# Kernel optimization log

Hardware: AMD Instinct MI355X
Metric: run time of the kernel (lower is better)

The kernel has to match this reference:

```python
import jax, jax.numpy as jnp
import numpy as np

B = 4096      # graphs
N = 21        # nodes per graph (EEG electrodes)
CIN = 512
H1 = 1024
H2 = 1024
COUT = 512
R = 4         # SE reduction
RANK = 10     # nodevec rank
EPS = 1e-5
THRESH = 0.1


def setup_inputs() -> dict:
    key = jax.random.key(0)
    ks = jax.random.split(key, 16)
    p = lambda i, shape, s=0.02: (jax.random.normal(ks[i], shape, jnp.float32) * s)
    return {
        "x": jax.random.normal(ks[0], (B * N, CIN), jnp.float32),
        "batch": jnp.arange(B * N, dtype=jnp.int32) // N,
        "nodevec1": jax.random.normal(ks[1], (N, RANK), jnp.float32),
        "nodevec2": jax.random.normal(ks[2], (RANK, N), jnp.float32),
        "se_w1": p(3, (CIN, CIN // R), 0.05),
        "se_w2": p(4, (CIN // R, CIN), 0.05),
        "W1": p(5, (CIN, H1)), "b1": jnp.zeros((H1,), jnp.float32),
        "W2": p(6, (H1, H2)), "b2": jnp.zeros((H2,), jnp.float32),
        "W3": p(7, (H2, COUT)), "b3": jnp.zeros((COUT,), jnp.float32),
        "bn1_g": jnp.ones((H1,), jnp.float32), "bn1_b": jnp.zeros((H1,), jnp.float32),
        "bn2_g": jnp.ones((H2,), jnp.float32), "bn2_b": jnp.zeros((H2,), jnp.float32),
        "bn3_g": jnp.ones((COUT,), jnp.float32), "bn3_b": jnp.zeros((COUT,), jnp.float32),
        "rs1_w": p(8, (CIN, H1)), "rs1_b": jnp.zeros((H1,), jnp.float32),
        "fc_w": p(9, (COUT, 2 * COUT)), "fc_b": jnp.zeros((2 * COUT,), jnp.float32),
    }


def _batchnorm(h, g, b):
    # training-mode BN: biased batch stats over the node dimension
    m = h.mean(0)
    v = h.var(0)
    return (h - m) * jax.lax.rsqrt(v + EPS) * g + b


def _gcn(A, h, W, b):
    # GCNConv with precomputed normalized+thresholded weights:
    # out = A_block_diag @ (h @ W) + b, done densely per graph since A is 21x21
    hm = (h @ W).reshape(B, N, -1)                 # [B, N, Cout]
    agg = jnp.einsum('ij,bjc->bic', A, hm)         # message passing per graph
    return agg.reshape(B * N, -1) + b


def _forward(x, batch, nodevec1, nodevec2, se_w1, se_w2,
             W1, b1, W2, b2, W3, b3,
             bn1_g, bn1_b, bn2_g, bn2_b, bn3_g, bn3_b,
             rs1_w, rs1_b, fc_w, fc_b):
    # SE layer on [B, N, C]: channel-wise gating from node-mean features
    x3 = x.reshape(B, N, CIN)
    y = jax.nn.sigmoid(jax.nn.relu(x3.mean(1) @ se_w1) @ se_w2)   # [B, C]
    xg = (x3 * y[:, None, :]).reshape(B * N, CIN)
    # adaptive adjacency: sigmoid(nv1 @ nv2), symmetric normalize, threshold
    adp = jax.nn.sigmoid(nodevec1 @ nodevec2)                      # [N, N]
    at = adp + jnp.eye(N, dtype=adp.dtype)
    deg = at.sum(1)
    dinv = jnp.where(deg > 0, deg ** -0.5, 0.0)
    A = dinv[:, None] * at * dinv[None, :]
    A = jnp.where(A > THRESH, A, 0.0)
    # layer 1 (+ projected residual, BN, relu; dropout omitted = eval)
    h = _batchnorm(_gcn(A, xg, W1, b1), bn1_g, bn1_b) + (xg @ rs1_w + rs1_b)
    h = jax.nn.relu(h)
    # layer 2 (h1 == h2 -> identity residual)
    h = jax.nn.relu(_batchnorm(_gcn(A, h, W2, b2), bn2_g, bn2_b) + h)
    # layer 3
    h = _batchnorm(_gcn(A, h, W3, b3), bn3_g, bn3_b)
    # global mean pool by graph id
    ssum = jax.ops.segment_sum(h, batch, num_segments=B)
    cnt = jax.ops.segment_sum(jnp.ones((h.shape[0], 1), h.dtype), batch, num_segments=B)
    pooled = ssum / cnt
    return pooled @ fc_w + fc_b                                    # [B, 2*COUT]


def reference(x, batch, nodevec1, nodevec2, se_w1, se_w2,
              W1, b1, W2, b2, W3, b3,
              bn1_g, bn1_b, bn2_g, bn2_b, bn3_g, bn3_b,
              rs1_w, rs1_b, fc_w, fc_b):
    return _forward(x, batch, nodevec1, nodevec2, se_w1, se_w2,
                    W1, b1, W2, b2, W3, b3,
                    bn1_g, bn1_b, bn2_g, bn2_b, bn3_g, bn3_b,
                    rs1_w, rs1_b, fc_w, fc_b)
```

## Files before the change

kernel.cpp:

```cpp
#include <hip/hip_runtime.h>

typedef _Float16 f16;
typedef f16 f16x2 __attribute__((ext_vector_type(2)));
typedef f16 f16x8 __attribute__((ext_vector_type(8)));
typedef float f32x4 __attribute__((ext_vector_type(4)));
typedef const void __attribute__((address_space(1)))* gas1;
typedef void __attribute__((address_space(3)))* las3;

#define NB 4096
#define NN 21
#define MROWS (NB*NN)
#define CIN 512

__global__ void k_adj(const float* __restrict__ nv1, const float* __restrict__ nv2,
                      float* __restrict__ Aout) {
  __shared__ float at[21][21];
  __shared__ float dinv[21];
  int t = threadIdx.x;
  if (t < 441) {
    int i = t / 21, j = t % 21;
    float s = 0.f;
    #pragma unroll
    for (int r = 0; r < 10; r++) s += nv1[i*10 + r] * nv2[r*21 + j];
    float v = 1.f / (1.f + expf(-s));
    if (i == j) v += 1.f;
    at[i][j] = v;
  }
  __syncthreads();
  if (t < 21) {
    float d = 0.f;
    #pragma unroll
    for (int j = 0; j < 21; j++) d += at[t][j];
    dinv[t] = d > 0.f ? rsqrtf(d) : 0.f;
  }
  __syncthreads();
  if (t < 441) {
    int i = t / 21, j = t % 21;
    float a = dinv[i] * at[i][j] * dinv[j];
    Aout[t] = a > 0.1f ? a : 0.f;
  }
}

__global__ void k_transpose(const float* __restrict__ src, f16* __restrict__ dst,
                            int K, int N) {
  __shared__ float tile[32][33];
  int n0 = blockIdx.x * 32, k0 = blockIdx.y * 32;
  int tx = threadIdx.x, ty = threadIdx.y;
  #pragma unroll
  for (int i = 0; i < 4; i++)
    tile[ty + 8*i][tx] = src[(size_t)(k0 + ty + 8*i) * N + n0 + tx];
  __syncthreads();
  #pragma unroll
  for (int i = 0; i < 4; i++)
    dst[(size_t)(n0 + ty + 8*i) * K + k0 + tx] = (f16)tile[tx][ty + 8*i];
}

__global__ void k_mean(const float* __restrict__ x, float* __restrict__ xm) {
  int b = blockIdx.x, t = threadIdx.x;
  for (int c = t; c < CIN; c += 256) {
    float s = 0.f;
    #pragma unroll
    for (int n = 0; n < NN; n++) s += x[((size_t)b*NN + n)*CIN + c];
    xm[(size_t)b*CIN + c] = s * (1.f/21.f);
  }
}

__global__ void k_se1(const float* __restrict__ xm, const float* __restrict__ w1,
                      float* __restrict__ y1) {
  __shared__ float row[CIN];
  int b = blockIdx.x, t = threadIdx.x;
  for (int k = t; k < CIN; k += 128) row[k] = xm[(size_t)b*CIN + k];
  __syncthreads();
  float acc = 0.f;
  for (int k = 0; k < CIN; k++) acc += row[k] * w1[(size_t)k*128 + t];
  y1[(size_t)b*128 + t] = fmaxf(acc, 0.f);
}

__global__ void k_se2(const float* __restrict__ y1, const float* __restrict__ w2,
                      float* __restrict__ y) {
  __shared__ float row[128];
  int b = blockIdx.x, t = threadIdx.x;
  if (t < 128) row[t] = y1[(size_t)b*128 + t];
  __syncthreads();
  float acc = 0.f;
  for (int k = 0; k < 128; k++) acc += row[k] * w2[(size_t)k*CIN + t];
  y[(size_t)b*CIN + t] = 1.f / (1.f + expf(-acc));
}

__global__ void k_gate(const float* __restrict__ x, const float* __restrict__ y,
                       f16* __restrict__ xg) {
  size_t i8 = (size_t)blockIdx.x * 256 + threadIdx.x;
  size_t base = i8 * 8;
  int r = (int)(base >> 9);
  int c = (int)(base & 511);
  int b = r / 21;
  const float4* xp = (const float4*)(x + base);
  const float4* yp = (const float4*)(y + (size_t)b*CIN + c);
  float4 a0 = xp[0], a1 = xp[1];
  float4 g0 = yp[0], g1 = yp[1];
  f16x8 o;
  o[0] = (f16)(a0.x * g0.x); o[1] = (f16)(a0.y * g0.y);
  o[2] = (f16)(a0.z * g0.z); o[3] = (f16)(a0.w * g0.w);
  o[4] = (f16)(a1.x * g1.x); o[5] = (f16)(a1.y * g1.y);
  o[6] = (f16)(a1.z * g1.z); o[7] = (f16)(a1.w * g1.w);
  *(f16x8*)(xg + base) = o;
}

#define GBM 128
#define GBN 256
#define BUFB 49152

template<int MODE>
__global__ __launch_bounds__(512, 1)
void k_gemm8(const f16* __restrict__ A, const f16* __restrict__ BT,
             f16* __restrict__ C1, const float* __restrict__ bias,
             float* __restrict__ Cf, float* __restrict__ psum,
             float* __restrict__ psq, int N, int K, int lgn) {
  __shared__ __align__(16) char lds[3 * BUFB];
  const int tid = threadIdx.x;
  const int nwg = gridDim.x;
  const int g = blockIdx.x;
  const int swz = (g & 7) * (nwg >> 3) + (g >> 3);
  const int bn = swz & ((1 << lgn) - 1);
  const int bm = swz >> lgn;
  const int lane = tid & 63;
  const int wid = tid >> 6;
  const int wr = wid >> 2;
  const int wc = wid & 3;
  const int fr = lane & 15;
  const int kg = lane >> 4;

  size_t srcOff[6]; int ldsOff[6];
  #pragma unroll
  for (int j = 0; j < 6; j++) {
    int gid = j * 512 + tid;
    if (gid < 1024) {
      int row = gid >> 3, gr = gid & 7;
      int gsw = gr ^ (row & 7);
      srcOff[j] = (size_t)(bm * GBM + row) * K + gsw * 8;
      ldsOff[j] = gid * 16;
    } else {
      int bgid = gid - 1024;
      int row = bgid >> 3, gr = bgid & 7;
      int gsw = gr ^ (row & 7);
      srcOff[j] = (size_t)(bn * GBN + row) * K + gsw * 8;
      ldsOff[j] = 16384 + bgid * 16;
    }
  }

  int aOff[4], axor[4], bOff[4], bxor[4];
  #pragma unroll
  for (int m = 0; m < 4; m++) {
    int row = wr*64 + m*16 + fr;
    aOff[m] = row * 128; axor[m] = row & 7;
  }
  #pragma unroll
  for (int n = 0; n < 4; n++) {
    int row = wc*64 + n*16 + fr;
    bOff[n] = 16384 + row * 128; bxor[n] = row & 7;
  }

  f32x4 acc[4][4];
  #pragma unroll
  for (int m = 0; m < 4; m++)
    #pragma unroll
    for (int n = 0; n < 4; n++)
      #pragma unroll
      for (int r = 0; r < 4; r++) acc[m][n][r] = 0.f;

  auto STAGE3 = [&](int t2, int sbuf, int j0) {
    char* dst = (char*)lds + sbuf * BUFB;
    const size_t kof = (size_t)t2 * 64;
    #pragma unroll
    for (int j = 0; j < 3; j++) {
      int jj = j0 + j;
      const f16* src = (jj < 2 ? A : BT) + srcOff[jj] + kof;
      __builtin_amdgcn_global_load_lds((gas1)src, (las3)(dst + ldsOff[jj]), 16, 0, 0);
    }
  };
  auto READF = [&](f16x8* avv, f16x8* bvv, const char* rb, int s) {
    #pragma unroll
    for (int m = 0; m < 4; m++)
      avv[m] = *(const f16x8*)(rb + aOff[m] + (((s*4 + kg) ^ axor[m]) << 4));
    #pragma unroll
    for (int n = 0; n < 4; n++)
      bvv[n] = *(const f16x8*)(rb + bOff[n] + (((s*4 + kg) ^ bxor[n]) << 4));
  };

  f16x8 av0[4], bv0[4], av1[4], bv1[4];
  const int NT = K >> 6;
  STAGE3(0, 0, 0); STAGE3(0, 0, 3);
  STAGE3(1, 1, 0); STAGE3(1, 1, 3);
  asm volatile("s_waitcnt vmcnt(6)" ::: "memory");
  asm volatile("s_barrier" ::: "memory");
  READF(av0, bv0, (const char*)lds, 0);

  for (int t = 0; t < NT; t++) {
    const char* rb  = (const char*)lds + (t % 3) * BUFB;
    const char* rbn = (const char*)lds + ((t + 1) % 3) * BUFB;
    const int sb = (t + 2) % 3;
    const bool stg  = (t + 2) < NT;
    const bool more = (t + 1) < NT;

    if (stg) STAGE3(t + 2, sb, 0);
    READF(av1, bv1, rb, 1);
    __builtin_amdgcn_s_setprio(1);
    #pragma unroll
    for (int m = 0; m < 4; m++)
      #pragma unroll
      for (int n = 0; n < 4; n++)
        acc[m][n] = __builtin_amdgcn_mfma_f32_16x16x32_f16(av0[m], bv0[n], acc[m][n], 0, 0, 0);
    __builtin_amdgcn_s_setprio(0);
    if (stg) STAGE3(t + 2, sb, 3);

    if (more) {
      if (stg) asm volatile("s_waitcnt vmcnt(6)" ::: "memory");
      else     asm volatile("s_waitcnt vmcnt(0)" ::: "memory");
      asm volatile("s_barrier" ::: "memory");
      READF(av0, bv0, rbn, 0);
    }
    __builtin_amdgcn_s_setprio(1);
    #pragma unroll
    for (int m = 0; m < 4; m++)
      #pragma unroll
      for (int n = 0; n < 4; n++)
        acc[m][n] = __builtin_amdgcn_mfma_f32_16x16x32_f16(av1[m], bv1[n], acc[m][n], 0, 0, 0);
    __builtin_amdgcn_s_setprio(0);
    asm volatile("s_barrier" ::: "memory");
  }

  const int crow = bm * GBM + wr * 64 + ((lane >> 4) << 2);
  const int ccol = bn * GBN + wc * 64 + fr;
  if constexpr (MODE == 2) {
    #pragma unroll
    for (int n = 0; n < 4; n++) {
      float bb = bias[ccol + n*16];
      #pragma unroll
      for (int m = 0; m < 4; m++)
        #pragma unroll
        for (int r = 0; r < 4; r++)
          Cf[(size_t)(crow + m*16 + r) * N + (ccol + n*16)] = acc[m][n][r] + bb;
    }
  } else {
    #pragma unroll
    for (int m = 0; m < 4; m++)
      #pragma unroll
      for (int n = 0; n < 4; n++)
        #pragma unroll
        for (int r = 0; r < 4; r++)
          C1[(size_t)(crow + m*16 + r) * N + (ccol + n*16)] = (f16)acc[m][n][r];
  }
  if constexpr (MODE == 1) {
    float s[4], q[4];
    #pragma unroll
    for (int n = 0; n < 4; n++) {
      float ss = 0.f, qq = 0.f;
      #pragma unroll
      for (int m = 0; m < 4; m++)
        #pragma unroll
        for (int r = 0; r < 4; r++) { float v = acc[m][n][r]; ss += v; qq = fmaf(v, v, qq); }
      s[n] = ss; q[n] = qq;
    }
    #pragma unroll
    for (int n = 0; n < 4; n++) {
      s[n] += __shfl_xor(s[n], 16); s[n] += __shfl_xor(s[n], 32);
      q[n] += __shfl_xor(q[n], 16); q[n] += __shfl_xor(q[n], 32);
    }
    float* wred = (float*)lds;
    if ((lane >> 4) == 0) {
      #pragma unroll
      for (int n = 0; n < 4; n++) {
        wred[wr*256 + wc*64 + n*16 + fr]       = s[n];
        wred[512 + wr*256 + wc*64 + n*16 + fr] = q[n];
      }
    }
    __syncthreads();
    if (tid < 256) {
      psum[(size_t)bm * N + bn*256 + tid] = wred[tid]       + wred[256 + tid];
      psq [(size_t)bm * N + bn*256 + tid] = wred[512 + tid] + wred[768 + tid];
    }
  }
}

__global__ __launch_bounds__(256)
void k_mixip(f16* __restrict__ t, const float* __restrict__ Aadj) {
  __shared__ float A[441];
  int b = blockIdx.x, tid = threadIdx.x;
  for (int i = tid; i < 441; i += 256) A[i] = Aadj[i];
  __syncthreads();
  int c0 = tid * 2;
  size_t base = (size_t)b * NN * 512 + c0;
  float vx[21], vy[21];
  #pragma unroll
  for (int j = 0; j < 21; j++) {
    f16x2 v = *(const f16x2*)(t + base + (size_t)j * 512);
    vx[j] = (float)v[0]; vy[j] = (float)v[1];
  }
  #pragma unroll
  for (int i = 0; i < 21; i++) {
    float a0 = 0.f, a1 = 0.f;
    #pragma unroll
    for (int j = 0; j < 21; j++) { float w = A[i*21+j]; a0 = fmaf(w, vx[j], a0); a1 = fmaf(w, vy[j], a1); }
    f16x2 o; o[0] = (f16)a0; o[1] = (f16)a1;
    *(f16x2*)(t + base + (size_t)i * 512) = o;
  }
}

__global__ __launch_bounds__(256)
void k_mix(f16* __restrict__ t, const float* __restrict__ Aadj,
           float* __restrict__ psum, float* __restrict__ psq, int C) {
  __shared__ float A[441];
  int b = blockIdx.x, tid = threadIdx.x;
  for (int i = tid; i < 441; i += 256) A[i] = Aadj[i];
  __syncthreads();
  int c0 = (blockIdx.y * 256 + tid) * 2;
  size_t base = (size_t)b * NN * C + c0;
  float vx[21], vy[21];
  #pragma unroll
  for (int j = 0; j < 21; j++) {
    f16x2 v = *(const f16x2*)(t + base + (size_t)j * C);
    vx[j] = (float)v[0]; vy[j] = (float)v[1];
  }
  float s0 = 0.f, s1 = 0.f, q0 = 0.f, q1 = 0.f;
  #pragma unroll
  for (int i = 0; i < 21; i++) {
    float a0 = 0.f, a1 = 0.f;
    #pragma unroll
    for (int j = 0; j < 21; j++) {
      float w = A[i*21 + j];
      a0 = fmaf(w, vx[j], a0);
      a1 = fmaf(w, vy[j], a1);
    }
    f16x2 o; o[0] = (f16)a0; o[1] = (f16)a1;
    *(f16x2*)(t + base + (size_t)i * C) = o;
    s0 += a0; s1 += a1;
    q0 = fmaf(a0, a0, q0); q1 = fmaf(a1, a1, q1);
  }
  float2 sv; sv.x = s0; sv.y = s1;
  float2 qv; qv.x = q0; qv.y = q1;
  *(float2*)(psum + (size_t)b * C + c0) = sv;
  *(float2*)(psq  + (size_t)b * C + c0) = qv;
}

__global__ void k_reduce(const float* __restrict__ ps, const float* __restrict__ pq,
                         float* __restrict__ rs, float* __restrict__ rq,
                         int C, int per) {
  int c = blockIdx.x * 256 + threadIdx.x;
  int py = blockIdx.y;
  float s = 0.f, q = 0.f;
  for (int p = py*per; p < py*per + per; p++) {
    s += ps[(size_t)p*C + c];
    q += pq[(size_t)p*C + c];
  }
  rs[(size_t)py*C + c] = s;
  rq[(size_t)py*C + c] = q;
}

__global__ void k_bnparams(const float* __restrict__ psum, const float* __restrict__ psq,
                           const float* __restrict__ gamma, const float* __restrict__ beta,
                           const float* __restrict__ resbias,
                           float* __restrict__ scale, float* __restrict__ shift,
                           int C, int npart) {
  int c = blockIdx.x * 256 + threadIdx.x;
  float s = 0.f, q = 0.f;
  for (int p = 0; p < npart; p++) { s += psum[(size_t)p*C + c]; q += psq[(size_t)p*C + c]; }
  const float Minv = 1.f / (float)MROWS;
  float mean = s * Minv;
  float var = q * Minv - mean * mean;
  float sc = gamma[c] * rsqrtf(var + 1e-5f);
  float sh = beta[c] - mean * sc;
  if (resbias) sh += resbias[c];
  scale[c] = sc; shift[c] = sh;
}

__global__ void k_finalize(const f16* __restrict__ g, const f16* res,
                           f16* dst, const float* __restrict__ scale,
                           const float* __restrict__ shift, int cmask) {
  size_t i8 = (size_t)blockIdx.x * 256 + threadIdx.x;
  size_t base = i8 * 8;
  int c = (int)(base & (size_t)cmask);
  f16x8 gv = *(const f16x8*)(g + base);
  f16x8 rv = *(const f16x8*)(res + base);
  f16x8 o;
  #pragma unroll
  for (int j = 0; j < 8; j++) {
    float v = (float)gv[j] * scale[c + j] + shift[c + j] + (float)rv[j];
    o[j] = (f16)fmaxf(v, 0.f);
  }
  *(f16x8*)(dst + base) = o;
}

__global__ __launch_bounds__(256)
void k_finmix(const f16* t, const f16* res, f16* hout, f16* hmix,
              const float* __restrict__ scale, const float* __restrict__ shift,
              const float* __restrict__ Aadj, int C) {
  __shared__ float A[441];
  int b = blockIdx.x, tid = threadIdx.x;
  for (int i = tid; i < 441; i += 256) A[i] = Aadj[i];
  __syncthreads();
  int c0 = (blockIdx.y * 256 + tid) * 2;
  float scx = scale[c0], scy = scale[c0+1];
  float shx = shift[c0], shy = shift[c0+1];
  size_t base = (size_t)b * NN * C + c0;
  float hx[21], hy[21];
  #pragma unroll
  for (int j = 0; j < 21; j++) {
    f16x2 tv = *(const f16x2*)(t + base + (size_t)j*C);
    f16x2 rv = *(const f16x2*)(res + base + (size_t)j*C);
    hx[j] = fmaxf((float)tv[0]*scx + shx + (float)rv[0], 0.f);
    hy[j] = fmaxf((float)tv[1]*scy + shy + (float)rv[1], 0.f);
    if (hout) {
      f16x2 o; o[0] = (f16)hx[j]; o[1] = (f16)hy[j];
      *(f16x2*)(hout + base + (size_t)j*C) = o;
    }
  }
  #pragma unroll
  for (int i = 0; i < 21; i++) {
    float a0 = 0.f, a1 = 0.f;
    #pragma unroll
    for (int j = 0; j < 21; j++) { float w = A[i*21+j]; a0 = fmaf(w, hx[j], a0); a1 = fmaf(w, hy[j], a1); }
    f16x2 o; o[0] = (f16)a0; o[1] = (f16)a1;
    *(f16x2*)(hmix + base + (size_t)i*C) = o;
  }
}

__global__ void k_pool(const f16* __restrict__ g3, const float* __restrict__ scale,
                       const float* __restrict__ shift, f16* __restrict__ pooled) {
  int b = blockIdx.x, t = threadIdx.x;
  for (int c = t; c < 512; c += 256) {
    float s = 0.f;
    #pragma unroll
    for (int n = 0; n < NN; n++) s += (float)g3[((size_t)b*NN + n)*512 + c];
    pooled[(size_t)b*512 + c] = (f16)((s * (1.f/21.f)) * scale[c] + shift[c]);
  }
}

extern "C" void kernel_launch(void* const* d_in, const int* in_sizes, int n_in,
                              void* d_out, int out_size, void* d_ws, size_t ws_size,
                              hipStream_t stream) {
  const float* x     = (const float*)d_in[0];
  const float* nv1   = (const float*)d_in[2];
  const float* nv2   = (const float*)d_in[3];
  const float* se_w1 = (const float*)d_in[4];
  const float* se_w2 = (const float*)d_in[5];
  const float* W1    = (const float*)d_in[6];
  const float* W2    = (const float*)d_in[8];
  const float* W3    = (const float*)d_in[10];
  const float* bn1g  = (const float*)d_in[12];
  const float* bn1b  = (const float*)d_in[13];
  const float* bn2g  = (const float*)d_in[14];
  const float* bn2b  = (const float*)d_in[15];
  const float* bn3g  = (const float*)d_in[16];
  const float* bn3b  = (const float*)d_in[17];
  const float* rs1w  = (const float*)d_in[18];
  const float* rs1b  = (const float*)d_in[19];
  const float* fcw   = (const float*)d_in[20];
  const float* fcb   = (const float*)d_in[21];
  float* out = (float*)d_out;

  char* ws = (char*)d_ws;
  size_t off = 0;
  auto alloc = [&](size_t bytes) -> char* {
    char* p = ws + off;
    off = (off + bytes + 255) & ~(size_t)255;
    return p;
  };

  float* A_adj = (float*)alloc(441 * 4);
  f16* W1T  = (f16*)alloc((size_t)1024 * 512 * 2);
  f16* RS1T = (f16*)alloc((size_t)1024 * 512 * 2);
  f16* W2T  = (f16*)alloc((size_t)1024 * 1024 * 2);
  f16* W3T  = (f16*)alloc((size_t)512 * 1024 * 2);
  f16* FCWT = (f16*)alloc((size_t)1024 * 512 * 2);
  float* psum = (float*)alloc((size_t)NB * 1024 * 4);
  float* psq  = (float*)alloc((size_t)NB * 1024 * 4);
  float* y1   = (float*)alloc((size_t)NB * 128 * 4);
  float* rsum = (float*)alloc((size_t)32 * 1024 * 4);
  float* rsq  = (float*)alloc((size_t)32 * 1024 * 4);
  float* sc1 = (float*)alloc(1024 * 4);
  float* sh1 = (float*)alloc(1024 * 4);
  float* sc2 = (float*)alloc(1024 * 4);
  float* sh2 = (float*)alloc(1024 * 4);
  float* sc3 = (float*)alloc(1024 * 4);
  float* sh3 = (float*)alloc(1024 * 4);
  f16* pooled = (f16*)alloc((size_t)NB * 512 * 2);
  f16* G = (f16*)alloc((size_t)MROWS * 512 * 2);
  f16* R = (f16*)alloc((size_t)MROWS * 1024 * 2);
  f16* T = (f16*)alloc((size_t)MROWS * 1024 * 2);
  float* xm = psum;
  float* yv = psq;
  (void)ws_size; (void)in_sizes; (void)n_in; (void)out_size;

  k_adj<<<1, 512, 0, stream>>>(nv1, nv2, A_adj);
  k_transpose<<<dim3(32, 16), dim3(32, 8), 0, stream>>>(W1,   W1T,  512, 1024);
  k_transpose<<<dim3(32, 16), dim3(32, 8), 0, stream>>>(rs1w, RS1T, 512, 1024);
  k_transpose<<<dim3(32, 32), dim3(32, 8), 0, stream>>>(W2,   W2T,  1024, 1024);
  k_transpose<<<dim3(16, 32), dim3(32, 8), 0, stream>>>(W3,   W3T,  1024, 512);
  k_transpose<<<dim3(32, 16), dim3(32, 8), 0, stream>>>(fcw,  FCWT, 512, 1024);

  k_mean<<<NB, 256, 0, stream>>>(x, xm);
  k_se1<<<NB, 128, 0, stream>>>(xm, se_w1, y1);
  k_se2<<<NB, 512, 0, stream>>>(y1, se_w2, yv);
  k_gate<<<21504, 256, 0, stream>>>(x, yv, G);

  k_gemm8<0><<<672*4, 512, 0, stream>>>(G, RS1T, R, nullptr, nullptr, nullptr, nullptr, 1024, 512, 2);
  k_mixip<<<NB, 256, 0, stream>>>(G, A_adj);
  k_gemm8<1><<<672*4, 512, 0, stream>>>(G, W1T, T, nullptr, nullptr, psum, psq, 1024, 512, 2);
  k_reduce<<<dim3(4, 32), 256, 0, stream>>>(psum, psq, rsum, rsq, 1024, 21);
  k_bnparams<<<4, 256, 0, stream>>>(rsum, rsq, bn1g, bn1b, rs1b, sc1, sh1, 1024, 32);
  k_finalize<<<43008, 256, 0, stream>>>(T, R, R, sc1, sh1, 1023);

  k_gemm8<0><<<672*4, 512, 0, stream>>>(R, W2T, T, nullptr, nullptr, nullptr, nullptr, 1024, 1024, 2);
  k_mix<<<dim3(NB, 2), 256, 0, stream>>>(T, A_adj, psum, psq, 1024);
  k_reduce<<<dim3(4, 32), 256, 0, stream>>>(psum, psq, rsum, rsq, 1024, 128);
  k_bnparams<<<4, 256, 0, stream>>>(rsum, rsq, bn2g, bn2b, nullptr, sc2, sh2, 1024, 32);
  k_finmix<<<dim3(NB, 2), 256, 0, stream>>>(T, R, nullptr, T, sc2, sh2, A_adj, 1024);

  k_gemm8<1><<<672*2, 512, 0, stream>>>(T, W3T, G, nullptr, nullptr, psum, psq, 512, 1024, 1);
  k_reduce<<<dim3(2, 32), 256, 0, stream>>>(psum, psq, rsum, rsq, 512, 21);
  k_bnparams<<<2, 256, 0, stream>>>(rsum, rsq, bn3g, bn3b, nullptr, sc3, sh3, 512, 32);

  k_pool<<<NB, 256, 0, stream>>>(G, sc3, sh3, pooled);
  k_gemm8<2><<<32*4, 512, 0, stream>>>(pooled, FCWT, nullptr, fcb, out, nullptr, nullptr, 1024, 512, 2);
}
```

Before: 1.186 ms.

## Shrink GEMM tiles to 128x128 with 4 waves, double buffering and two workgroups per CU

The f16 MFMA GEMM changes from a 128x256 tile run by 8 waves with a triple-buffered LDS pipeline and one workgroup per CU to a 128x128 tile run by 4 waves. It uses a 64 KB double buffer and launch bounds that allow two workgroups per CU. The aim is to let co-resident workgroups hide each other's load and barrier stalls and to balance the grid better. In exchange, each tile reuses operands less, and each k-step now waits for all outstanding loads, so the pipeline inside a workgroup is shallower. The grid sizes, swizzle shift and BN partial-sum reduction layout are adjusted to the new tile width.

Result: slower. 1.214 ms (+2.4%).

```diff
diff --git a/kernel.cpp b/kernel.cpp
--- a/kernel.cpp
+++ b/kernel.cpp
@@ -107,16 +107,16 @@
 }
 
 #define GBM 128
-#define GBN 256
-#define BUFB 49152
+#define GBN 128
+#define HBUF 32768
 
 template<int MODE>
-__global__ __launch_bounds__(512, 1)
-void k_gemm8(const f16* __restrict__ A, const f16* __restrict__ BT,
+__global__ __launch_bounds__(256, 2)
+void k_gemm4(const f16* __restrict__ A, const f16* __restrict__ BT,
              f16* __restrict__ C1, const float* __restrict__ bias,
              float* __restrict__ Cf, float* __restrict__ psum,
              float* __restrict__ psq, int N, int K, int lgn) {
-  __shared__ __align__(16) char lds[3 * BUFB];
+  __shared__ __align__(16) char lds[2 * HBUF];
   const int tid = threadIdx.x;
   const int nwg = gridDim.x;
   const int g = blockIdx.x;
@@ -125,26 +125,24 @@
   const int bm = swz >> lgn;
   const int lane = tid & 63;
   const int wid = tid >> 6;
-  const int wr = wid >> 2;
-  const int wc = wid & 3;
+  const int wr = wid >> 1;
+  const int wc = wid & 1;
   const int fr = lane & 15;
   const int kg = lane >> 4;
 
-  size_t srcOff[6]; int ldsOff[6];
-  #pragma unroll
-  for (int j = 0; j < 6; j++) {
-    int gid = j * 512 + tid;
+  size_t srcOff[8]; int ldsOff[8];
+  #pragma unroll
+  for (int j = 0; j < 8; j++) {
+    int gid = j * 256 + tid;
+    int row = (gid >> 3) & 127;
+    int gr = gid & 7;
+    int gsw = gr ^ (row & 7);
     if (gid < 1024) {
-      int row = gid >> 3, gr = gid & 7;
-      int gsw = gr ^ (row & 7);
       srcOff[j] = (size_t)(bm * GBM + row) * K + gsw * 8;
       ldsOff[j] = gid * 16;
     } else {
-      int bgid = gid - 1024;
-      int row = bgid >> 3, gr = bgid & 7;
-      int gsw = gr ^ (row & 7);
       srcOff[j] = (size_t)(bn * GBN + row) * K + gsw * 8;
-      ldsOff[j] = 16384 + bgid * 16;
+      ldsOff[j] = 16384 + (gid - 1024) * 16;
     }
   }
 
@@ -168,14 +166,13 @@
       #pragma unroll
       for (int r = 0; r < 4; r++) acc[m][n][r] = 0.f;
 
-  auto STAGE3 = [&](int t2, int sbuf, int j0) {
-    char* dst = (char*)lds + sbuf * BUFB;
+  auto STAGE8 = [&](int t2, int sbuf) {
+    char* dst = (char*)lds + sbuf * HBUF;
     const size_t kof = (size_t)t2 * 64;
     #pragma unroll
-    for (int j = 0; j < 3; j++) {
-      int jj = j0 + j;
-      const f16* src = (jj < 2 ? A : BT) + srcOff[jj] + kof;
-      __builtin_amdgcn_global_load_lds((gas1)src, (las3)(dst + ldsOff[jj]), 16, 0, 0);
+    for (int j = 0; j < 8; j++) {
+      const f16* src = (j < 4 ? A : BT) + srcOff[j] + kof;
+      __builtin_amdgcn_global_load_lds((gas1)src, (las3)(dst + ldsOff[j]), 16, 0, 0);
     }
   };
   auto READF = [&](f16x8* avv, f16x8* bvv, const char* rb, int s) {
@@ -189,20 +186,17 @@
 
   f16x8 av0[4], bv0[4], av1[4], bv1[4];
   const int NT = K >> 6;
-  STAGE3(0, 0, 0); STAGE3(0, 0, 3);
-  STAGE3(1, 1, 0); STAGE3(1, 1, 3);
-  asm volatile("s_waitcnt vmcnt(6)" ::: "memory");
+  STAGE8(0, 0);
+  asm volatile("s_waitcnt vmcnt(0)" ::: "memory");
   asm volatile("s_barrier" ::: "memory");
   READF(av0, bv0, (const char*)lds, 0);
 
   for (int t = 0; t < NT; t++) {
-    const char* rb  = (const char*)lds + (t % 3) * BUFB;
-    const char* rbn = (const char*)lds + ((t + 1) % 3) * BUFB;
-    const int sb = (t + 2) % 3;
-    const bool stg  = (t + 2) < NT;
-    const bool more = (t + 1) < NT;
-
-    if (stg) STAGE3(t + 2, sb, 0);
+    const char* rb  = (const char*)lds + (t & 1) * HBUF;
+    const char* rbn = (const char*)lds + ((t + 1) & 1) * HBUF;
+    const bool stg = (t + 1) < NT;
+
+    if (stg) STAGE8(t + 1, (t + 1) & 1);
     READF(av1, bv1, rb, 1);
     __builtin_amdgcn_s_setprio(1);
     #pragma unroll
@@ -211,14 +205,9 @@
       for (int n = 0; n < 4; n++)
         acc[m][n] = __builtin_amdgcn_mfma_f32_16x16x32_f16(av0[m], bv0[n], acc[m][n], 0, 0, 0);
     __builtin_amdgcn_s_setprio(0);
-    if (stg) STAGE3(t + 2, sb, 3);
-
-    if (more) {
-      if (stg) asm volatile("s_waitcnt vmcnt(6)" ::: "memory");
-      else     asm volatile("s_waitcnt vmcnt(0)" ::: "memory");
-      asm volatile("s_barrier" ::: "memory");
-      READF(av0, bv0, rbn, 0);
-    }
+    if (stg) asm volatile("s_waitcnt vmcnt(0)" ::: "memory");
+    asm volatile("s_barrier" ::: "memory");
+    if (stg) READF(av0, bv0, rbn, 0);
     __builtin_amdgcn_s_setprio(1);
     #pragma unroll
     for (int m = 0; m < 4; m++)
@@ -226,7 +215,6 @@
       for (int n = 0; n < 4; n++)
         acc[m][n] = __builtin_amdgcn_mfma_f32_16x16x32_f16(av1[m], bv1[n], acc[m][n], 0, 0, 0);
     __builtin_amdgcn_s_setprio(0);
-    asm volatile("s_barrier" ::: "memory");
   }
 
   const int crow = bm * GBM + wr * 64 + ((lane >> 4) << 2);
@@ -267,17 +255,18 @@
       q[n] += __shfl_xor(q[n], 16); q[n] += __shfl_xor(q[n], 32);
     }
     float* wred = (float*)lds;
+    __syncthreads();
     if ((lane >> 4) == 0) {
       #pragma unroll
       for (int n = 0; n < 4; n++) {
-        wred[wr*256 + wc*64 + n*16 + fr]       = s[n];
-        wred[512 + wr*256 + wc*64 + n*16 + fr] = q[n];
+        wred[wr*128 + wc*64 + n*16 + fr]       = s[n];
+        wred[256 + wr*128 + wc*64 + n*16 + fr] = q[n];
       }
     }
     __syncthreads();
-    if (tid < 256) {
-      psum[(size_t)bm * N + bn*256 + tid] = wred[tid]       + wred[256 + tid];
-      psq [(size_t)bm * N + bn*256 + tid] = wred[512 + tid] + wred[768 + tid];
+    if (tid < 128) {
+      psum[(size_t)bm * N + bn*128 + tid] = wred[tid]       + wred[128 + tid];
+      psq [(size_t)bm * N + bn*128 + tid] = wred[256 + tid] + wred[384 + tid];
     }
   }
 }
@@ -503,23 +492,23 @@
   k_se2<<<NB, 512, 0, stream>>>(y1, se_w2, yv);
   k_gate<<<21504, 256, 0, stream>>>(x, yv, G);
 
-  k_gemm8<0><<<672*4, 512, 0, stream>>>(G, RS1T, R, nullptr, nullptr, nullptr, nullptr, 1024, 512, 2);
+  k_gemm4<0><<<672*8, 256, 0, stream>>>(G, RS1T, R, nullptr, nullptr, nullptr, nullptr, 1024, 512, 3);
   k_mixip<<<NB, 256, 0, stream>>>(G, A_adj);
-  k_gemm8<1><<<672*4, 512, 0, stream>>>(G, W1T, T, nullptr, nullptr, psum, psq, 1024, 512, 2);
+  k_gemm4<1><<<672*8, 256, 0, stream>>>(G, W1T, T, nullptr, nullptr, psum, psq, 1024, 512, 3);
   k_reduce<<<dim3(4, 32), 256, 0, stream>>>(psum, psq, rsum, rsq, 1024, 21);
   k_bnparams<<<4, 256, 0, stream>>>(rsum, rsq, bn1g, bn1b, rs1b, sc1, sh1, 1024, 32);
   k_finalize<<<43008, 256, 0, stream>>>(T, R, R, sc1, sh1, 1023);
 
-  k_gemm8<0><<<672*4, 512, 0, stream>>>(R, W2T, T, nullptr, nullptr, nullptr, nullptr, 1024, 1024, 2);
+  k_gemm4<0><<<672*8, 256, 0, stream>>>(R, W2T, T, nullptr, nullptr, nullptr, nullptr, 1024, 1024, 3);
   k_mix<<<dim3(NB, 2), 256, 0, stream>>>(T, A_adj, psum, psq, 1024);
   k_reduce<<<dim3(4, 32), 256, 0, stream>>>(psum, psq, rsum, rsq, 1024, 128);
   k_bnparams<<<4, 256, 0, stream>>>(rsum, rsq, bn2g, bn2b, nullptr, sc2, sh2, 1024, 32);
   k_finmix<<<dim3(NB, 2), 256, 0, stream>>>(T, R, nullptr, T, sc2, sh2, A_adj, 1024);
 
-  k_gemm8<1><<<672*2, 512, 0, stream>>>(T, W3T, G, nullptr, nullptr, psum, psq, 512, 1024, 1);
+  k_gemm4<1><<<672*4, 256, 0, stream>>>(T, W3T, G, nullptr, nullptr, psum, psq, 512, 1024, 2);
   k_reduce<<<dim3(2, 32), 256, 0, stream>>>(psum, psq, rsum, rsq, 512, 21);
   k_bnparams<<<2, 256, 0, stream>>>(rsum, rsq, bn3g, bn3b, nullptr, sc3, sh3, 512, 32);
 
   k_pool<<<NB, 256, 0, stream>>>(G, sc3, sh3, pooled);
-  k_gemm8<2><<<32*4, 512, 0, stream>>>(pooled, FCWT, nullptr, fcb, out, nullptr, nullptr, 1024, 512, 2);
-}
+  k_gemm4<2><<<32*8, 256, 0, stream>>>(pooled, FCWT, nullptr, fcb, out, nullptr, nullptr, 1024, 512, 3);
+}
```
